# Performance work log

Measured on AMD Instinct MI355X. Metric: run time of the kernel, lower is better.

## Reference

```python
import jax, jax.numpy as jnp
import numpy as np

B, D, H, E, NDIFF = 4096, 2048, 4096, 8, 3
TOPK = 2


def setup_inputs() -> dict:
    key = jax.random.key(0)
    ks = jax.random.split(key, 8)
    x = jax.random.normal(ks[0], (B, D), dtype=jnp.float32)
    difficulty_labels = jax.random.randint(ks[1], (B,), 0, NDIFF)
    emb = jax.random.normal(ks[2], (NDIFF, D), dtype=jnp.float32) * 0.02
    gate_W = jax.random.normal(ks[3], (E, 2 * D), dtype=jnp.float32) / np.sqrt(2.0 * D)
    gate_b = jnp.zeros((E,), dtype=jnp.float32)
    expert_W = jax.random.normal(ks[4], (E, H, D), dtype=jnp.float32) / np.sqrt(D)
    expert_b = jax.random.normal(ks[5], (E, H), dtype=jnp.float32) * 0.01
    return {"x": x, "difficulty_labels": difficulty_labels, "emb": emb,
            "gate_W": gate_W, "gate_b": gate_b,
            "expert_W": expert_W, "expert_b": expert_b}


def reference(x, difficulty_labels, emb, gate_W, gate_b, expert_W, expert_b):
    # gating: concat token features with difficulty embedding
    gate_in = jnp.concatenate([x, emb[difficulty_labels]], axis=1)       # [B, 2D]
    gate_logits = gate_in @ gate_W.T + gate_b                             # [B, E]
    topw, topk_idx = jax.lax.top_k(gate_logits, TOPK)                     # [B, 2]
    topk_probs = jax.nn.softmax(topw, axis=1)                             # [B, 2]
    # per-token combine weight for each expert (top-2 indices are distinct)
    combine = jnp.zeros((x.shape[0], E), dtype=x.dtype)
    combine = combine.at[jnp.arange(x.shape[0])[:, None], topk_idx].add(topk_probs)
    # dispatch/compute/combine: tokens with combine weight 0 contribute 0,
    # matching the masked gather/scatter-add of the original.
    out = jnp.zeros((x.shape[0], expert_W.shape[1]), dtype=x.dtype)
    for e in range(E):  # small fixed loop over experts
        y = x @ expert_W[e].T + expert_b[e]                               # [B, H]
        out = out + y * combine[:, e:e + 1]
    return (out, topk_idx)
```

## Files before the change

kernel.cpp:

```cpp
#include <hip/hip_runtime.h>
#include <hip/hip_bf16.h>

#define B_TOK 4096
#define DIM   2048
#define HID   4096
#define NEXP  8
#define CAP   4224

#define BM 128
#define BN 128
#define BK 32
#define KITER (DIM / BK)

typedef short  bf16x8 __attribute__((ext_vector_type(8)));
typedef unsigned short us16x8 __attribute__((ext_vector_type(8)));
typedef float  f32x4  __attribute__((ext_vector_type(4)));

__device__ __forceinline__ unsigned short f2bf(float f) {
    unsigned u = __builtin_bit_cast(unsigned, f);
    u += 0x7fffu + ((u >> 16) & 1u);
    return (unsigned short)(u >> 16);
}

__device__ __forceinline__ void async_copy16(const void* g, void* l) {
    __builtin_amdgcn_global_load_lds(
        (const __attribute__((address_space(1))) unsigned*)g,
        (__attribute__((address_space(3))) unsigned*)l, 16, 0, 0);
}

__global__ __launch_bounds__(256) void cvt_kernel(
    const float* __restrict__ src, unsigned short* __restrict__ dst, long n) {
    long i = ((long)blockIdx.x * 256 + threadIdx.x) * 8;
    if (i >= n) return;
    float4 v0 = *(const float4*)(src + i);
    float4 v1 = *(const float4*)(src + i + 4);
    us16x8 o = { f2bf(v0.x), f2bf(v0.y), f2bf(v0.z), f2bf(v0.w),
                 f2bf(v1.x), f2bf(v1.y), f2bf(v1.z), f2bf(v1.w) };
    *(us16x8*)(dst + i) = o;
}

__global__ __launch_bounds__(256) void compute_c_kernel(
    const float* __restrict__ emb, const float* __restrict__ gate_W,
    const float* __restrict__ gate_b, float* __restrict__ cbuf) {
    int wave = (blockIdx.x * blockDim.x + threadIdx.x) >> 6;
    int lane = threadIdx.x & 63;
    if (wave >= 24) return;
    int n = wave >> 3, e = wave & 7;
    const float4* er = (const float4*)(emb + (size_t)n * DIM);
    const float4* wr = (const float4*)(gate_W + (size_t)e * 2 * DIM + DIM);
    float acc = 0.f;
    for (int c = lane; c < DIM / 4; c += 64) {
        float4 a = er[c], b = wr[c];
        acc += a.x * b.x + a.y * b.y + a.z * b.z + a.w * b.w;
    }
    #pragma unroll
    for (int off = 32; off; off >>= 1) acc += __shfl_down(acc, off, 64);
    if (lane == 0) cbuf[n * 8 + e] = acc + gate_b[e];
}

__global__ __launch_bounds__(256) void gating_kernel(
    const float* __restrict__ x, const int* __restrict__ labels,
    const float* __restrict__ gate_W, const float* __restrict__ cbuf,
    int* __restrict__ counts, int* __restrict__ tlist, int* __restrict__ rlist,
    float* __restrict__ wA, float* __restrict__ wB,
    int* __restrict__ eA, int* __restrict__ eB,
    unsigned short* __restrict__ xb, float* __restrict__ out_idx) {
    int wave = threadIdx.x >> 6, lane = threadIdx.x & 63;
    int b = blockIdx.x * 4 + wave;
    const float4* xr  = (const float4*)(x + (size_t)b * DIM);
    const float4* gw4 = (const float4*)gate_W;
    unsigned short* xo = xb + (size_t)b * DIM;
    float acc[8] = {0.f, 0.f, 0.f, 0.f, 0.f, 0.f, 0.f, 0.f};
    for (int c = lane; c < DIM / 4; c += 64) {
        float4 xv = xr[c];
        ushort4 xc = { f2bf(xv.x), f2bf(xv.y), f2bf(xv.z), f2bf(xv.w) };
        *(ushort4*)(xo + 4 * c) = xc;
        #pragma unroll
        for (int e = 0; e < 8; ++e) {
            float4 wv = gw4[e * (2 * DIM / 4) + c];
            acc[e] += xv.x * wv.x + xv.y * wv.y + xv.z * wv.z + xv.w * wv.w;
        }
    }
    #pragma unroll
    for (int off = 32; off; off >>= 1) {
        #pragma unroll
        for (int e = 0; e < 8; ++e) acc[e] += __shfl_down(acc[e], off, 64);
    }
    if (lane == 0) {
        int lbl = labels[b];
        float lg[8];
        #pragma unroll
        for (int e = 0; e < 8; ++e) lg[e] = acc[e] + cbuf[lbl * 8 + e];
        int e0 = 0; float t0 = lg[0];
        #pragma unroll
        for (int e = 1; e < 8; ++e) if (lg[e] > t0) { t0 = lg[e]; e0 = e; }
        int e1 = -1; float t1 = -1e30f;
        #pragma unroll
        for (int e = 0; e < 8; ++e)
            if (e != e0 && lg[e] > t1) { t1 = lg[e]; e1 = e; }
        float w0 = 1.f / (1.f + __expf(t1 - t0));
        float w1 = 1.f - w0;
        int p0 = atomicAdd(&counts[e0], 1);
        int p1 = atomicAdd(&counts[e1], 1);
        tlist[e0 * CAP + p0] = b; rlist[e0 * CAP + p0] = 0;
        tlist[e1 * CAP + p1] = b; rlist[e1 * CAP + p1] = 1;
        wA[b] = w0; wB[b] = w1; eA[b] = e0; eB[b] = e1;
        out_idx[2 * b]     = (float)e0;
        out_idx[2 * b + 1] = (float)e1;
    }
}

__global__ void pad_kernel(const int* __restrict__ counts,
                           int* __restrict__ tlist, int* __restrict__ rlist) {
    int e = blockIdx.x, c = counts[e];
    int padded = (c + BM - 1) & ~(BM - 1);
    int i = c + threadIdx.x;
    if (i < padded) { tlist[e * CAP + i] = 0; rlist[e * CAP + i] = 2; }
}

__global__ __launch_bounds__(256, 3) void moe_gemm_kernel(
    const unsigned short* __restrict__ xb, const unsigned short* __restrict__ Wb,
    const int* __restrict__ counts, const int* __restrict__ tlist,
    const int* __restrict__ rlist,
    float* __restrict__ out0, float* __restrict__ y1, float* __restrict__ trash) {
    const int e  = blockIdx.z;
    const int m0 = blockIdx.y * BM;
    if (m0 >= counts[e]) return;
    const int n0 = blockIdx.x * BN;

    __shared__ unsigned short As0[BM * BK], As1[BM * BK];
    __shared__ unsigned short Bs0[BN * BK], Bs1[BN * BK];
    __shared__ int toks[BM];
    __shared__ unsigned long long rowp[BM];

    const int t = threadIdx.x;
    if (t < BM) {
        int tok = tlist[e * CAP + m0 + t];
        int rk  = rlist[e * CAP + m0 + t];
        toks[t] = tok;
        float* p = (rk == 0) ? out0 + (size_t)tok * HID
                 : (rk == 1) ? y1   + (size_t)tok * HID
                             : trash;
        rowp[t] = (unsigned long long)p;
    }
    __syncthreads();

    const int lane = t & 63, wave = t >> 6;
    const int rowc = lane >> 2;
    const int colg = lane & 3;
    const int gcol = ((colg ^ ((rowc >> 1) & 3)) * 8);

    const unsigned short* gA[2];
    const unsigned short* gB[2];
    int ldsoff[2];
    #pragma unroll
    for (int j = 0; j < 2; ++j) {
        int row = wave * 32 + j * 16 + rowc;
        gA[j] = xb + (size_t)toks[row] * DIM + gcol;
        gB[j] = Wb + ((size_t)e * HID + n0 + row) * DIM + gcol;
        ldsoff[j] = (wave * 32 + j * 16) * BK;
    }

    const int wm = wave >> 1, wn = wave & 1;
    const int r = lane & 15, quad = lane >> 4;
    const int pg = ((quad ^ ((r >> 1) & 3)) * 8);

    f32x4 acc[4][4] = {};

    auto stage = [&](unsigned short* Ad, unsigned short* Bd, int kstep) {
        const int kc = kstep * BK;
        #pragma unroll
        for (int j = 0; j < 2; ++j) {
            async_copy16(gA[j] + kc, Ad + ldsoff[j]);
            async_copy16(gB[j] + kc, Bd + ldsoff[j]);
        }
    };
    auto compute = [&](const unsigned short* Ab, const unsigned short* Bb) {
        bf16x8 af[4], bfr[4];
        #pragma unroll
        for (int i = 0; i < 4; ++i) {
            af[i]  = *(const bf16x8*)&Ab[(wm * 64 + i * 16 + r) * BK + pg];
            bfr[i] = *(const bf16x8*)&Bb[(wn * 64 + i * 16 + r) * BK + pg];
        }
        #pragma unroll
        for (int im = 0; im < 4; ++im)
            #pragma unroll
            for (int in = 0; in < 4; ++in)
                acc[im][in] = __builtin_amdgcn_mfma_f32_16x16x32_bf16(
                    af[im], bfr[in], acc[im][in], 0, 0, 0);
    };

    stage(As0, Bs0, 0);
    __syncthreads();
    for (int k2 = 0; k2 < KITER; k2 += 2) {
        stage(As1, Bs1, k2 + 1);
        compute(As0, Bs0);
        __syncthreads();
        if (k2 + 2 < KITER) stage(As0, Bs0, k2 + 2);
        compute(As1, Bs1);
        __syncthreads();
    }

    #pragma unroll
    for (int in = 0; in < 4; ++in) {
        int col = n0 + wn * 64 + in * 16 + r;
        #pragma unroll
        for (int im = 0; im < 4; ++im) {
            int rowb = wm * 64 + im * 16 + quad * 4;
            #pragma unroll
            for (int r4 = 0; r4 < 4; ++r4) {
                float* dst = (float*)rowp[rowb + r4];
                dst[col] = acc[im][in][r4];
            }
        }
    }
}

__global__ __launch_bounds__(256) void combine_kernel(
    const float* __restrict__ y1, const float* __restrict__ eb,
    const float* __restrict__ wA, const float* __restrict__ wB,
    const int* __restrict__ eA, const int* __restrict__ eB,
    float* __restrict__ out) {
    int b = blockIdx.x;
    float w0 = wA[b], w1 = wB[b];
    int e0 = eA[b], e1 = eB[b];
    const float4* y0r = (const float4*)(out + (size_t)b * HID);
    const float4* y1r = (const float4*)(y1 + (size_t)b * HID);
    const float4* b0r = (const float4*)(eb + (size_t)e0 * HID);
    const float4* b1r = (const float4*)(eb + (size_t)e1 * HID);
    float4* o = (float4*)(out + (size_t)b * HID);
    for (int i = threadIdx.x; i < HID / 4; i += 256) {
        float4 a = y0r[i], c = y1r[i], u = b0r[i], v = b1r[i];
        float4 rs;
        rs.x = w0 * (a.x + u.x) + w1 * (c.x + v.x);
        rs.y = w0 * (a.y + u.y) + w1 * (c.y + v.y);
        rs.z = w0 * (a.z + u.z) + w1 * (c.z + v.z);
        rs.w = w0 * (a.w + u.w) + w1 * (c.w + v.w);
        o[i] = rs;
    }
}

extern "C" void kernel_launch(void* const* d_in, const int* in_sizes, int n_in,
                              void* d_out, int out_size, void* d_ws, size_t ws_size,
                              hipStream_t stream) {
    const float* x        = (const float*)d_in[0];
    const int*   labels   = (const int*)  d_in[1];
    const float* emb      = (const float*)d_in[2];
    const float* gate_W   = (const float*)d_in[3];
    const float* gate_b   = (const float*)d_in[4];
    const float* expert_W = (const float*)d_in[5];
    const float* expert_b = (const float*)d_in[6];
    float* out = (float*)d_out;

    char* ws = (char*)d_ws;
    int*   counts = (int*)ws;
    float* cbuf   = (float*)(ws + 256);
    int*   tlist  = (int*)(ws + 512);
    int*   rlist  = (int*)(ws + 512 + 135168);
    float* wA     = (float*)(ws + 270848);
    float* wB     = (float*)(ws + 287232);
    int*   eA     = (int*)  (ws + 303616);
    int*   eB     = (int*)  (ws + 320000);
    float* trash  = (float*)(ws + 336384);
    float* y1     = (float*)(ws + 352768);
    unsigned short* xb = (unsigned short*)(ws + 352768 + (size_t)B_TOK * HID * 4);
    unsigned short* Wb = xb + (size_t)B_TOK * DIM;

    hipMemsetAsync(counts, 0, 8 * sizeof(int), stream);

    cvt_kernel<<<(NEXP * HID * DIM) / (8 * 256), 256, 0, stream>>>(
        expert_W, Wb, (long)NEXP * HID * DIM);
    compute_c_kernel<<<6, 256, 0, stream>>>(emb, gate_W, gate_b, cbuf);
    gating_kernel<<<B_TOK / 4, 256, 0, stream>>>(
        x, labels, gate_W, cbuf, counts, tlist, rlist, wA, wB, eA, eB, xb,
        out + (size_t)B_TOK * HID);
    pad_kernel<<<NEXP, BM, 0, stream>>>(counts, tlist, rlist);
    moe_gemm_kernel<<<dim3(HID / BN, B_TOK / BM, NEXP), 256, 0, stream>>>(
        xb, Wb, counts, tlist, rlist, out, y1, trash);
    combine_kernel<<<B_TOK, 256, 0, stream>>>(
        y1, expert_b, wA, wB, eA, eB, out);
}
```

Baseline: 746.2 us.

## Enlarge MoE GEMM tile to 256x256x64 with 8 waves and phased ping-pong pipeline

The grouped expert GEMM moves from 128x128x32 tiles with 4 waves to 256x256x64 tiles with 8 waves per block. The K-loop is split into fine-grained phases that interleave async global-to-LDS copies with MFMA work, using explicit barriers, vmcnt waits, sched_barrier and setprio. The aim is higher data reuse per block and better overlap of loads with matrix math. In exchange, per-expert padding waste grows with BM=256, capacity and workspace offsets change, and register and LDS pressure rise.

```diff
diff --git a/kernel.cpp b/kernel.cpp
--- a/kernel.cpp
+++ b/kernel.cpp
@@ -5,12 +5,12 @@
 #define DIM   2048
 #define HID   4096
 #define NEXP  8
-#define CAP   4224
-
-#define BM 128
-#define BN 128
-#define BK 32
-#define KITER (DIM / BK)
+#define CAP   4352
+
+#define BM 256
+#define BN 256
+#define BK 64
+#define KIT (DIM / BK)
 
 typedef short  bf16x8 __attribute__((ext_vector_type(8)));
 typedef unsigned short us16x8 __attribute__((ext_vector_type(8)));
@@ -118,7 +118,53 @@
     if (i < padded) { tlist[e * CAP + i] = 0; rlist[e * CAP + i] = 2; }
 }
 
-__global__ __launch_bounds__(256, 3) void moe_gemm_kernel(
+#define STAGE_A(BUF, KS, KT) do {                                        \
+    const int _off = (KT) * BK + (KS) * 32;                              \
+    async_copy16(gA0 + _off, &Ab[BUF][KS][ldsA0]);                       \
+    async_copy16(gA1 + _off, &Ab[BUF][KS][ldsA1]);                       \
+} while (0)
+
+#define STAGE_B(BUF, KS, KT) do {                                        \
+    const int _off = (KT) * BK + (KS) * 32;                              \
+    async_copy16(gB0 + _off, &Bb[BUF][KS][ldsA0]);                       \
+    async_copy16(gB1 + _off, &Bb[BUF][KS][ldsA1]);                       \
+} while (0)
+
+#define PHASE(BUF, MH, KS, LOADB, STAGE_STMT, WAITN) do {                \
+    const unsigned short* _As = Ab[BUF][KS];                             \
+    const unsigned short* _Bs = Bb[BUF][KS];                             \
+    bf16x8 _a[4];                                                        \
+    _Pragma("unroll")                                                    \
+    for (int fi = 0; fi < 4; ++fi)                                       \
+        _a[fi] = *(const bf16x8*)                                        \
+            &_As[(wm * 128 + (MH) * 64 + fi * 16 + r) * 32 + fsw];       \
+    if (LOADB) {                                                         \
+        _Pragma("unroll")                                                \
+        for (int nf = 0; nf < 4; ++nf)                                   \
+            bfr[nf] = *(const bf16x8*)                                   \
+                &_Bs[(wn * 64 + nf * 16 + r) * 32 + fsw];                \
+    }                                                                    \
+    STAGE_STMT;                                                          \
+    asm volatile("" ::: "memory");                                       \
+    __builtin_amdgcn_s_barrier();                                        \
+    __builtin_amdgcn_sched_barrier(0);                                   \
+    __builtin_amdgcn_s_setprio(1);                                       \
+    _Pragma("unroll")                                                    \
+    for (int fi = 0; fi < 4; ++fi)                                       \
+        _Pragma("unroll")                                                \
+        for (int nf = 0; nf < 4; ++nf)                                   \
+            acc[(MH) * 4 + fi][nf] =                                     \
+                __builtin_amdgcn_mfma_f32_16x16x32_bf16(                 \
+                    _a[fi], bfr[nf], acc[(MH) * 4 + fi][nf], 0, 0, 0);   \
+    __builtin_amdgcn_s_setprio(0);                                       \
+    if ((WAITN) == 4)      asm volatile("s_waitcnt vmcnt(4)" ::: "memory"); \
+    else if ((WAITN) == 0) asm volatile("s_waitcnt vmcnt(0)" ::: "memory"); \
+    else                   asm volatile("" ::: "memory");                \
+    __builtin_amdgcn_s_barrier();                                        \
+    __builtin_amdgcn_sched_barrier(0);                                   \
+} while (0)
+
+__global__ __launch_bounds__(512, 2) void moe_gemm_kernel(
     const unsigned short* __restrict__ xb, const unsigned short* __restrict__ Wb,
     const int* __restrict__ counts, const int* __restrict__ tlist,
     const int* __restrict__ rlist,
@@ -128,8 +174,8 @@
     if (m0 >= counts[e]) return;
     const int n0 = blockIdx.x * BN;
 
-    __shared__ unsigned short As0[BM * BK], As1[BM * BK];
-    __shared__ unsigned short Bs0[BN * BK], Bs1[BN * BK];
+    __shared__ unsigned short Ab[2][2][256 * 32];
+    __shared__ unsigned short Bb[2][2][256 * 32];
     __shared__ int toks[BM];
     __shared__ unsigned long long rowp[BM];
 
@@ -145,72 +191,64 @@
     }
     __syncthreads();
 
-    const int lane = t & 63, wave = t >> 6;
-    const int rowc = lane >> 2;
-    const int colg = lane & 3;
-    const int gcol = ((colg ^ ((rowc >> 1) & 3)) * 8);
-
-    const unsigned short* gA[2];
-    const unsigned short* gB[2];
-    int ldsoff[2];
+    const int lane = t & 63, wv = t >> 6;
+    const int r = lane & 15, quad = lane >> 4;
+    const int wm = wv >> 2, wn = wv & 3;
+    const int fsw = (quad ^ ((r >> 1) & 3)) * 8;
+
+    const unsigned short *gA0, *gA1, *gB0, *gB1;
+    int ldsA0, ldsA1;
+    {
+        int c0 = t,      row0 = c0 >> 2, ls0 = (c0 & 3) ^ ((row0 >> 1) & 3);
+        int c1 = t + 512, row1 = c1 >> 2, ls1 = (c1 & 3) ^ ((row1 >> 1) & 3);
+        gA0 = xb + (size_t)toks[row0] * DIM + ls0 * 8;
+        gA1 = xb + (size_t)toks[row1] * DIM + ls1 * 8;
+        gB0 = Wb + ((size_t)e * HID + n0 + row0) * DIM + ls0 * 8;
+        gB1 = Wb + ((size_t)e * HID + n0 + row1) * DIM + ls1 * 8;
+        ldsA0 = (wv * 64) * 8;
+        ldsA1 = (512 + wv * 64) * 8;
+    }
+
+    f32x4 acc[8][4] = {};
+    bf16x8 bfr[4];
+
+    STAGE_A(0, 0, 0); STAGE_B(0, 0, 0); STAGE_A(0, 1, 0); STAGE_B(0, 1, 0);
+    asm volatile("s_waitcnt vmcnt(4)" ::: "memory");
+    __builtin_amdgcn_s_barrier();
+    __builtin_amdgcn_sched_barrier(0);
+
+    for (int k2 = 0; k2 < KIT; k2 += 2) {
+        {
+            const int nt = k2 + 1;
+            PHASE(0, 0, 0, 1, STAGE_A(1, 0, nt), -1);
+            PHASE(0, 1, 0, 0, STAGE_B(1, 0, nt),  4);
+            PHASE(0, 0, 1, 1, STAGE_A(1, 1, nt), -1);
+            PHASE(0, 1, 1, 0, STAGE_B(1, 1, nt),  4);
+        }
+        if (k2 + 2 < KIT) {
+            const int nt = k2 + 2;
+            PHASE(1, 0, 0, 1, STAGE_A(0, 0, nt), -1);
+            PHASE(1, 1, 0, 0, STAGE_B(0, 0, nt),  4);
+            PHASE(1, 0, 1, 1, STAGE_A(0, 1, nt), -1);
+            PHASE(1, 1, 1, 0, STAGE_B(0, 1, nt),  4);
+        } else {
+            PHASE(1, 0, 0, 1, ((void)0), -1);
+            PHASE(1, 1, 0, 0, ((void)0),  0);
+            PHASE(1, 0, 1, 1, ((void)0), -1);
+            PHASE(1, 1, 1, 0, ((void)0), -1);
+        }
+    }
+
     #pragma unroll
-    for (int j = 0; j < 2; ++j) {
-        int row = wave * 32 + j * 16 + rowc;
-        gA[j] = xb + (size_t)toks[row] * DIM + gcol;
-        gB[j] = Wb + ((size_t)e * HID + n0 + row) * DIM + gcol;
-        ldsoff[j] = (wave * 32 + j * 16) * BK;
-    }
-
-    const int wm = wave >> 1, wn = wave & 1;
-    const int r = lane & 15, quad = lane >> 4;
-    const int pg = ((quad ^ ((r >> 1) & 3)) * 8);
-
-    f32x4 acc[4][4] = {};
-
-    auto stage = [&](unsigned short* Ad, unsigned short* Bd, int kstep) {
-        const int kc = kstep * BK;
-        #pragma unroll
-        for (int j = 0; j < 2; ++j) {
-            async_copy16(gA[j] + kc, Ad + ldsoff[j]);
-            async_copy16(gB[j] + kc, Bd + ldsoff[j]);
-        }
-    };
-    auto compute = [&](const unsigned short* Ab, const unsigned short* Bb) {
-        bf16x8 af[4], bfr[4];
-        #pragma unroll
-        for (int i = 0; i < 4; ++i) {
-            af[i]  = *(const bf16x8*)&Ab[(wm * 64 + i * 16 + r) * BK + pg];
-            bfr[i] = *(const bf16x8*)&Bb[(wn * 64 + i * 16 + r) * BK + pg];
-        }
-        #pragma unroll
-        for (int im = 0; im < 4; ++im)
-            #pragma unroll
-            for (int in = 0; in < 4; ++in)
-                acc[im][in] = __builtin_amdgcn_mfma_f32_16x16x32_bf16(
-                    af[im], bfr[in], acc[im][in], 0, 0, 0);
-    };
-
-    stage(As0, Bs0, 0);
-    __syncthreads();
-    for (int k2 = 0; k2 < KITER; k2 += 2) {
-        stage(As1, Bs1, k2 + 1);
-        compute(As0, Bs0);
-        __syncthreads();
-        if (k2 + 2 < KITER) stage(As0, Bs0, k2 + 2);
-        compute(As1, Bs1);
-        __syncthreads();
-    }
-
-    #pragma unroll
-    for (int in = 0; in < 4; ++in) {
-        int col = n0 + wn * 64 + in * 16 + r;
-        #pragma unroll
-        for (int im = 0; im < 4; ++im) {
-            int rowb = wm * 64 + im * 16 + quad * 4;
+    for (int nf = 0; nf < 4; ++nf) {
+        int col = n0 + wn * 64 + nf * 16 + r;
+        #pragma unroll
+        for (int mi = 0; mi < 8; ++mi) {
+            int rowb = wm * 128 + mi * 16 + quad * 4;
             #pragma unroll
             for (int r4 = 0; r4 < 4; ++r4) {
                 float* dst = (float*)rowp[rowb + r4];
-                dst[col] = acc[im][in][r4];
+                dst[col] = acc[mi][nf][r4];
             }
         }
     }
@@ -256,14 +294,14 @@
     int*   counts = (int*)ws;
     float* cbuf   = (float*)(ws + 256);
     int*   tlist  = (int*)(ws + 512);
-    int*   rlist  = (int*)(ws + 512 + 135168);
-    float* wA     = (float*)(ws + 270848);
-    float* wB     = (float*)(ws + 287232);
-    int*   eA     = (int*)  (ws + 303616);
-    int*   eB     = (int*)  (ws + 320000);
-    float* trash  = (float*)(ws + 336384);
-    float* y1     = (float*)(ws + 352768);
-    unsigned short* xb = (unsigned short*)(ws + 352768 + (size_t)B_TOK * HID * 4);
+    int*   rlist  = (int*)(ws + 512 + 139264);
+    float* wA     = (float*)(ws + 279040);
+    float* wB     = (float*)(ws + 295424);
+    int*   eA     = (int*)  (ws + 311808);
+    int*   eB     = (int*)  (ws + 328192);
+    float* trash  = (float*)(ws + 344576);
+    float* y1     = (float*)(ws + 360960);
+    unsigned short* xb = (unsigned short*)(ws + 360960 + (size_t)B_TOK * HID * 4);
     unsigned short* Wb = xb + (size_t)B_TOK * DIM;
 
     hipMemsetAsync(counts, 0, 8 * sizeof(int), stream);
@@ -274,8 +312,8 @@
     gating_kernel<<<B_TOK / 4, 256, 0, stream>>>(
         x, labels, gate_W, cbuf, counts, tlist, rlist, wA, wB, eA, eB, xb,
         out + (size_t)B_TOK * HID);
-    pad_kernel<<<NEXP, BM, 0, stream>>>(counts, tlist, rlist);
-    moe_gemm_kernel<<<dim3(HID / BN, B_TOK / BM, NEXP), 256, 0, stream>>>(
+    pad_kernel<<<NEXP, 256, 0, stream>>>(counts, tlist, rlist);
+    moe_gemm_kernel<<<dim3(HID / BN, B_TOK / BM, NEXP), 512, 0, stream>>>(
         xb, Wb, counts, tlist, rlist, out, y1, trash);
     combine_kernel<<<B_TOK, 256, 0, stream>>>(
         y1, expert_b, wA, wB, eA, eB, out);
```

Measured after the change: 1.329 ms. 78.1% more time.

## Fuse expert combine into GEMM epilogue via weighted atomic adds

Applied to the files above, without the earlier changes.

Removes the separate combine kernel and the y1 scratch buffer. The GEMM epilogue now adds the expert bias, scales by the gating weight and atomically accumulates into a zeroed output, so each token's two expert contributions sum in place. This saves a full write and read of the 64MB intermediate, but adds a memset of the output and scalar float atomics in the epilogue. The change also raises the GEMM occupancy hint from 3 to 4 and turns the conversion kernel into a grid-stride loop with fewer blocks.

```diff
diff --git a/kernel.cpp b/kernel.cpp
--- a/kernel.cpp
+++ b/kernel.cpp
@@ -30,13 +30,14 @@
 
 __global__ __launch_bounds__(256) void cvt_kernel(
     const float* __restrict__ src, unsigned short* __restrict__ dst, long n) {
-    long i = ((long)blockIdx.x * 256 + threadIdx.x) * 8;
-    if (i >= n) return;
-    float4 v0 = *(const float4*)(src + i);
-    float4 v1 = *(const float4*)(src + i + 4);
-    us16x8 o = { f2bf(v0.x), f2bf(v0.y), f2bf(v0.z), f2bf(v0.w),
-                 f2bf(v1.x), f2bf(v1.y), f2bf(v1.z), f2bf(v1.w) };
-    *(us16x8*)(dst + i) = o;
+    long stride = (long)gridDim.x * 256 * 8;
+    for (long i = ((long)blockIdx.x * 256 + threadIdx.x) * 8; i < n; i += stride) {
+        float4 v0 = *(const float4*)(src + i);
+        float4 v1 = *(const float4*)(src + i + 4);
+        us16x8 o = { f2bf(v0.x), f2bf(v0.y), f2bf(v0.z), f2bf(v0.w),
+                     f2bf(v1.x), f2bf(v1.y), f2bf(v1.z), f2bf(v1.w) };
+        *(us16x8*)(dst + i) = o;
+    }
 }
 
 __global__ __launch_bounds__(256) void compute_c_kernel(
@@ -63,7 +64,6 @@
     const float* __restrict__ gate_W, const float* __restrict__ cbuf,
     int* __restrict__ counts, int* __restrict__ tlist, int* __restrict__ rlist,
     float* __restrict__ wA, float* __restrict__ wB,
-    int* __restrict__ eA, int* __restrict__ eB,
     unsigned short* __restrict__ xb, float* __restrict__ out_idx) {
     int wave = threadIdx.x >> 6, lane = threadIdx.x & 63;
     int b = blockIdx.x * 4 + wave;
@@ -104,7 +104,7 @@
         int p1 = atomicAdd(&counts[e1], 1);
         tlist[e0 * CAP + p0] = b; rlist[e0 * CAP + p0] = 0;
         tlist[e1 * CAP + p1] = b; rlist[e1 * CAP + p1] = 1;
-        wA[b] = w0; wB[b] = w1; eA[b] = e0; eB[b] = e1;
+        wA[b] = w0; wB[b] = w1;
         out_idx[2 * b]     = (float)e0;
         out_idx[2 * b + 1] = (float)e1;
     }
@@ -118,11 +118,12 @@
     if (i < padded) { tlist[e * CAP + i] = 0; rlist[e * CAP + i] = 2; }
 }
 
-__global__ __launch_bounds__(256, 3) void moe_gemm_kernel(
+__global__ __launch_bounds__(256, 4) void moe_gemm_kernel(
     const unsigned short* __restrict__ xb, const unsigned short* __restrict__ Wb,
     const int* __restrict__ counts, const int* __restrict__ tlist,
-    const int* __restrict__ rlist,
-    float* __restrict__ out0, float* __restrict__ y1, float* __restrict__ trash) {
+    const int* __restrict__ rlist, const float* __restrict__ wA,
+    const float* __restrict__ wB, const float* __restrict__ eb,
+    float* __restrict__ out) {
     const int e  = blockIdx.z;
     const int m0 = blockIdx.y * BM;
     if (m0 >= counts[e]) return;
@@ -130,18 +131,15 @@
 
     __shared__ unsigned short As0[BM * BK], As1[BM * BK];
     __shared__ unsigned short Bs0[BN * BK], Bs1[BN * BK];
-    __shared__ int toks[BM];
-    __shared__ unsigned long long rowp[BM];
+    __shared__ int   toks[BM];
+    __shared__ float roww[BM];
 
     const int t = threadIdx.x;
     if (t < BM) {
         int tok = tlist[e * CAP + m0 + t];
         int rk  = rlist[e * CAP + m0 + t];
         toks[t] = tok;
-        float* p = (rk == 0) ? out0 + (size_t)tok * HID
-                 : (rk == 1) ? y1   + (size_t)tok * HID
-                             : trash;
-        rowp[t] = (unsigned long long)p;
+        roww[t] = (rk == 0) ? wA[tok] : (rk == 1) ? wB[tok] : 0.f;
     }
     __syncthreads();
 
@@ -204,39 +202,18 @@
     #pragma unroll
     for (int in = 0; in < 4; ++in) {
         int col = n0 + wn * 64 + in * 16 + r;
+        float bc = eb[(size_t)e * HID + col];
         #pragma unroll
         for (int im = 0; im < 4; ++im) {
             int rowb = wm * 64 + im * 16 + quad * 4;
             #pragma unroll
             for (int r4 = 0; r4 < 4; ++r4) {
-                float* dst = (float*)rowp[rowb + r4];
-                dst[col] = acc[im][in][r4];
+                float w = roww[rowb + r4];
+                if (w != 0.f)
+                    atomicAdd(out + (size_t)toks[rowb + r4] * HID + col,
+                              w * (acc[im][in][r4] + bc));
             }
         }
-    }
-}
-
-__global__ __launch_bounds__(256) void combine_kernel(
-    const float* __restrict__ y1, const float* __restrict__ eb,
-    const float* __restrict__ wA, const float* __restrict__ wB,
-    const int* __restrict__ eA, const int* __restrict__ eB,
-    float* __restrict__ out) {
-    int b = blockIdx.x;
-    float w0 = wA[b], w1 = wB[b];
-    int e0 = eA[b], e1 = eB[b];
-    const float4* y0r = (const float4*)(out + (size_t)b * HID);
-    const float4* y1r = (const float4*)(y1 + (size_t)b * HID);
-    const float4* b0r = (const float4*)(eb + (size_t)e0 * HID);
-    const float4* b1r = (const float4*)(eb + (size_t)e1 * HID);
-    float4* o = (float4*)(out + (size_t)b * HID);
-    for (int i = threadIdx.x; i < HID / 4; i += 256) {
-        float4 a = y0r[i], c = y1r[i], u = b0r[i], v = b1r[i];
-        float4 rs;
-        rs.x = w0 * (a.x + u.x) + w1 * (c.x + v.x);
-        rs.y = w0 * (a.y + u.y) + w1 * (c.y + v.y);
-        rs.z = w0 * (a.z + u.z) + w1 * (c.z + v.z);
-        rs.w = w0 * (a.w + u.w) + w1 * (c.w + v.w);
-        o[i] = rs;
     }
 }
 
@@ -259,24 +236,19 @@
     int*   rlist  = (int*)(ws + 512 + 135168);
     float* wA     = (float*)(ws + 270848);
     float* wB     = (float*)(ws + 287232);
-    int*   eA     = (int*)  (ws + 303616);
-    int*   eB     = (int*)  (ws + 320000);
-    float* trash  = (float*)(ws + 336384);
-    float* y1     = (float*)(ws + 352768);
-    unsigned short* xb = (unsigned short*)(ws + 352768 + (size_t)B_TOK * HID * 4);
+    unsigned short* xb = (unsigned short*)(ws + 303616);
     unsigned short* Wb = xb + (size_t)B_TOK * DIM;
 
     hipMemsetAsync(counts, 0, 8 * sizeof(int), stream);
-
-    cvt_kernel<<<(NEXP * HID * DIM) / (8 * 256), 256, 0, stream>>>(
+    hipMemsetAsync(out, 0, (size_t)B_TOK * HID * sizeof(float), stream);
+
+    cvt_kernel<<<4096, 256, 0, stream>>>(
         expert_W, Wb, (long)NEXP * HID * DIM);
     compute_c_kernel<<<6, 256, 0, stream>>>(emb, gate_W, gate_b, cbuf);
     gating_kernel<<<B_TOK / 4, 256, 0, stream>>>(
-        x, labels, gate_W, cbuf, counts, tlist, rlist, wA, wB, eA, eB, xb,
+        x, labels, gate_W, cbuf, counts, tlist, rlist, wA, wB, xb,
         out + (size_t)B_TOK * HID);
     pad_kernel<<<NEXP, BM, 0, stream>>>(counts, tlist, rlist);
     moe_gemm_kernel<<<dim3(HID / BN, B_TOK / BM, NEXP), 256, 0, stream>>>(
-        xb, Wb, counts, tlist, rlist, out, y1, trash);
-    combine_kernel<<<B_TOK, 256, 0, stream>>>(
-        y1, expert_b, wA, wB, eA, eB, out);
-}
+        xb, Wb, counts, tlist, rlist, wA, wB, expert_b, out);
+}
```

Result: slower. 831.4 us (+11.4%).
